# Kernel optimization log

Measured on AMD Instinct MI355X. Metric: run time of the kernel, lower is better.

## Reference

```python
import jax, jax.numpy as jnp
import numpy as np

N = 50000
IN_FEATS = 128
H_FEATS = 256
E = 800000


def setup_inputs() -> dict:
    key = jax.random.key(0)
    ks = jax.random.split(key, 8)
    x = jax.random.normal(ks[0], (N, IN_FEATS), dtype=jnp.float32)
    edge_index = jax.random.randint(ks[1], (2, E), 0, N, dtype=jnp.int64)
    s1 = 1.0 / np.sqrt(IN_FEATS)
    s2 = 1.0 / np.sqrt(H_FEATS)
    # PyG SAGEConv: lin_l (applied to aggregated neighbors, with bias), lin_r (root, no bias)
    W1_l = jax.random.uniform(ks[2], (H_FEATS, IN_FEATS), jnp.float32, -s1, s1)
    b1_l = jax.random.uniform(ks[3], (H_FEATS,), jnp.float32, -s1, s1)
    W1_r = jax.random.uniform(ks[4], (H_FEATS, IN_FEATS), jnp.float32, -s1, s1)
    W2_l = jax.random.uniform(ks[5], (1, H_FEATS), jnp.float32, -s2, s2)
    b2_l = jax.random.uniform(ks[6], (1,), jnp.float32, -s2, s2)
    W2_r = jax.random.uniform(ks[7], (1, H_FEATS), jnp.float32, -s2, s2)
    return {"x": x, "edge_index": edge_index, "W1_l": W1_l, "b1_l": b1_l,
            "W1_r": W1_r, "W2_l": W2_l, "b2_l": b2_l, "W2_r": W2_r}


def _mean_aggregate(feat, src, dst, n_nodes):
    # scatter-mean of source features onto destination nodes
    summed = jax.ops.segment_sum(feat[src], dst, num_segments=n_nodes)
    deg = jax.ops.segment_sum(jnp.ones((src.shape[0],), feat.dtype), dst,
                              num_segments=n_nodes)
    return summed / jnp.maximum(deg, 1.0)[:, None]


def reference(x, edge_index, W1_l, b1_l, W1_r, W2_l, b2_l, W2_r):
    src, dst = edge_index[0], edge_index[1]
    n = x.shape[0]
    # SAGEConv 1: lin_l(mean_agg(x)) + lin_r(x), then ReLU (dropout is identity at eval)
    agg1 = _mean_aggregate(x, src, dst, n)
    h = jax.nn.relu(agg1 @ W1_l.T + b1_l + x @ W1_r.T)
    # SAGEConv 2 -> scalar per node
    agg2 = _mean_aggregate(h, src, dst, n)
    out = (agg2 @ W2_l.T + b2_l + h @ W2_r.T).reshape(-1)
    return out
```

## Files before the change

### kernel.cpp

```cpp
#include <hip/hip_runtime.h>

static constexpr int IN_F   = 128;
static constexpr int ECH    = 4096;
static constexpr int RSLOT  = 64;
static constexpr int CAPB   = 5376;
static constexpr int CSR_CAP = 5376;
static constexpr int OVF_CAP = 4096;

typedef __attribute__((ext_vector_type(8))) short bf16x8;
typedef __attribute__((ext_vector_type(8))) unsigned short u16x8;
typedef __attribute__((ext_vector_type(4))) float f32x4;

__device__ inline unsigned short f2bf(float f) {
    unsigned u = __float_as_uint(f);
    u += 0x7FFF + ((u >> 16) & 1);
    return (unsigned short)(u >> 16);
}
__device__ inline float bf2f(unsigned short h) {
    return __uint_as_float(((unsigned)h) << 16);
}

__global__ __launch_bounds__(256) void edge_bin(const int* __restrict__ src,
        const int* __restrict__ dst, unsigned* __restrict__ btmp,
        int* __restrict__ rcnt, int* __restrict__ ovf_cnt, unsigned* __restrict__ ovf,
        int E) {
    __shared__ unsigned stage[ECH];
    __shared__ int h[256], lcur[256];
    int tid = threadIdx.x, eb = blockIdx.x;
    int base = eb * ECH;
    h[tid] = 0; lcur[tid] = 0;
    __syncthreads();
#pragma unroll
    for (int r = 0; r < ECH / 256; r++) {
        int e = base + r * 256 + tid;
        if (e < E) {
            unsigned d = (unsigned)dst[e];
            stage[r * 256 + tid] = (d << 16) | (unsigned)src[e];
            atomicAdd(&h[d >> 8], 1);
        }
    }
    __syncthreads();
    int hv = h[tid];
    rcnt[eb * 256 + tid] = hv < RSLOT ? hv : RSLOT;
#pragma unroll
    for (int r = 0; r < ECH / 256; r++) {
        int e = base + r * 256 + tid;
        if (e < E) {
            unsigned pk = stage[r * 256 + tid];
            int bkt = pk >> 24;
            int rank = atomicAdd(&lcur[bkt], 1);
            if (rank < RSLOT)
                btmp[(size_t)(eb * 256 + bkt) * RSLOT + rank] = pk;
            else {
                int pos = atomicAdd(ovf_cnt, 1);
                if (pos < OVF_CAP) ovf[pos] = pk;
            }
        }
    }
}

__global__ __launch_bounds__(256) void bucket_csr(const unsigned* __restrict__ btmp,
        const int* __restrict__ rcnt, const int* __restrict__ ovf_cnt,
        const unsigned* __restrict__ ovf,
        int* __restrict__ rowbeg, int* __restrict__ degn, int* __restrict__ col,
        int n, int nblk) {
    __shared__ unsigned stage[CSR_CAP];
    __shared__ unsigned colL[CSR_CAP];
    __shared__ int cntL[256], curL[256];
    __shared__ int ws[4];
    __shared__ int s_extra;
    int b = blockIdx.x, tid = threadIdx.x, lane = tid & 63, wid = tid >> 6;

    int rc = (tid < nblk) ? rcnt[tid * 256 + b] : 0;
    int val = rc;
#pragma unroll
    for (int off = 1; off < 64; off <<= 1) {
        int t = __shfl_up(val, off);
        if (lane >= off) val += t;
    }
    if (lane == 63) ws[wid] = val;
    if (tid == 0) s_extra = 0;
    cntL[tid] = 0;
    __syncthreads();
    int pre = 0;
    for (int w = 0; w < wid; w++) pre += ws[w];
    int rb  = pre + val - rc;
    int cnt = ws[0] + ws[1] + ws[2] + ws[3];
    if (tid < nblk && rc > 0) {
        const unsigned* sp = btmp + (size_t)(tid * 256 + b) * RSLOT;
        for (int i = 0; i < rc; i++) stage[rb + i] = sp[i];
    }
    __syncthreads();
    int novf = *ovf_cnt;
    if (novf > 0) {
        if (novf > OVF_CAP) novf = OVF_CAP;
        for (int i = tid; i < novf; i += 256) {
            unsigned pk = ovf[i];
            if ((int)(pk >> 24) == b) {
                int pos = atomicAdd(&s_extra, 1);
                if (cnt + pos < CSR_CAP) stage[cnt + pos] = pk;
            }
        }
    }
    __syncthreads();
    cnt += s_extra;
    if (cnt > CSR_CAP) cnt = CSR_CAP;
    for (int i = tid; i < cnt; i += 256) atomicAdd(&cntL[(stage[i] >> 16) & 255], 1);
    __syncthreads();
    int v = cntL[tid];
    int val2 = v;
#pragma unroll
    for (int off = 1; off < 64; off <<= 1) {
        int t = __shfl_up(val2, off);
        if (lane >= off) val2 += t;
    }
    if (lane == 63) ws[wid] = val2;
    __syncthreads();
    pre = 0;
    for (int w = 0; w < wid; w++) pre += ws[w];
    int ex = pre + val2 - v;
    curL[tid] = ex;
    int node = b * 256 + tid;
    if (node < n) { rowbeg[node] = b * CAPB + ex; degn[node] = v; }
    __syncthreads();
    for (int i = tid; i < cnt; i += 256) {
        unsigned pk = stage[i];
        int pos = atomicAdd(&curL[(pk >> 16) & 255], 1);
        colL[pos] = pk & 0xFFFFu;
    }
    __syncthreads();
    for (int i = tid; i < cnt; i += 256) col[b * CAPB + i] = (int)colL[i];
}

__global__ __launch_bounds__(256) void split_xw(const float* __restrict__ x,
        const float* __restrict__ W1l, const float* __restrict__ W1r,
        unsigned short* __restrict__ xh,
        unsigned short* __restrict__ Wh, unsigned short* __restrict__ Wl,
        long long total2) {
    long long i = (long long)blockIdx.x * 256 + threadIdx.x;
    if (i < total2) {
        float2 v = ((const float2*)x)[i];
        ((ushort2*)xh)[i] = make_ushort2(f2bf(v.x), f2bf(v.y));
    } else {
        long long wi = i - total2;
        if (wi < 65536) {
            int feat = (int)(wi >> 8), k = (int)(wi & 255);
            float w = (k < IN_F) ? W1l[feat * IN_F + k] : W1r[feat * IN_F + (k - IN_F)];
            unsigned short h = f2bf(w);
            Wh[wi] = h;
            Wl[wi] = f2bf(w - bf2f(h));
        }
    }
}

__global__ void agg1_kernel(const unsigned short* __restrict__ xh,
                            const int* __restrict__ rowbeg, const int* __restrict__ degn,
                            const int* __restrict__ col,
                            unsigned short* __restrict__ aggh, int n) {
    int gid  = blockIdx.x * blockDim.x + threadIdx.x;
    int node = gid >> 5;
    int l32  = threadIdx.x & 31;
    if (node >= n) return;
    int beg = rowbeg[node], dg = degn[node], end = beg + dg;
    float a0 = 0.f, a1 = 0.f, a2 = 0.f, a3 = 0.f;
    int j = beg;
    for (; j + 3 < end; j += 4) {
        int4 cs = *(const int4*)(col + j);
        ushort4 v0 = ((const ushort4*)(xh + (size_t)cs.x * IN_F))[l32];
        ushort4 v1 = ((const ushort4*)(xh + (size_t)cs.y * IN_F))[l32];
        ushort4 v2 = ((const ushort4*)(xh + (size_t)cs.z * IN_F))[l32];
        ushort4 v3 = ((const ushort4*)(xh + (size_t)cs.w * IN_F))[l32];
        a0 += bf2f(v0.x) + bf2f(v1.x) + bf2f(v2.x) + bf2f(v3.x);
        a1 += bf2f(v0.y) + bf2f(v1.y) + bf2f(v2.y) + bf2f(v3.y);
        a2 += bf2f(v0.z) + bf2f(v1.z) + bf2f(v2.z) + bf2f(v3.z);
        a3 += bf2f(v0.w) + bf2f(v1.w) + bf2f(v2.w) + bf2f(v3.w);
    }
    for (; j < end; j++) {
        ushort4 v0 = ((const ushort4*)(xh + (size_t)col[j] * IN_F))[l32];
        a0 += bf2f(v0.x); a1 += bf2f(v0.y); a2 += bf2f(v0.z); a3 += bf2f(v0.w);
    }
    float inv = 1.0f / fmaxf((float)dg, 1.0f);
    ushort4 hi;
    hi.x = f2bf(a0 * inv); hi.y = f2bf(a1 * inv);
    hi.z = f2bf(a2 * inv); hi.w = f2bf(a3 * inv);
    ((ushort4*)(aggh + (size_t)node * IN_F))[l32] = hi;
}

__global__ __launch_bounds__(256, 2) void layer1_kernel(
        const unsigned short* __restrict__ xh,
        const unsigned short* __restrict__ aggh,
        const unsigned short* __restrict__ Wh, const unsigned short* __restrict__ Wl,
        const float* __restrict__ b1l,
        const float* __restrict__ W2l, const float* __restrict__ W2r,
        float* __restrict__ p, float* __restrict__ q, int n) {
    __shared__ unsigned short Ah[128 * 32];
    __shared__ unsigned short Bh[256 * 32];
    __shared__ unsigned short Bl[256 * 32];

    int tid  = threadIdx.x;
    int lane = tid & 63;
    int wv   = tid >> 6;
    int m15  = lane & 15;
    int quad = lane >> 4;
    int node0 = blockIdx.x * 128;

    f32x4 acc[2][16];
#pragma unroll
    for (int nt = 0; nt < 2; nt++)
#pragma unroll
        for (int ft = 0; ft < 16; ft++) acc[nt][ft] = (f32x4){0.f, 0.f, 0.f, 0.f};

    int rown = tid >> 2;
    int sub  = tid & 3;

    for (int kc = 0; kc < 8; kc++) {
        int k0 = kc * 32;
        const unsigned short* Ahs = (kc < 4) ? aggh : xh;
        int aoff = (kc < 4) ? k0 : (k0 - IN_F);

#pragma unroll
        for (int ps = 0; ps < 2; ps++) {
            int nl = ps * 64 + rown;
            int g  = node0 + nl;
            u16x8 hv = {0,0,0,0,0,0,0,0};
            if (g < n) hv = *(const u16x8*)(Ahs + (size_t)g * IN_F + aoff + sub * 8);
            *(u16x8*)&Ah[nl * 32 + sub * 8] = hv;
        }
#pragma unroll
        for (int ps = 0; ps < 4; ps++) {
            int feat = ps * 64 + rown;
            size_t go = (size_t)feat * 256 + k0 + sub * 8;
            *(u16x8*)&Bh[feat * 32 + sub * 8] = *(const u16x8*)(Wh + go);
            *(u16x8*)&Bl[feat * 32 + sub * 8] = *(const u16x8*)(Wl + go);
        }
        __syncthreads();

        bf16x8 a0h = *(const bf16x8*)&Ah[(wv * 32 + m15) * 32 + quad * 8];
        bf16x8 a1h = *(const bf16x8*)&Ah[(wv * 32 + 16 + m15) * 32 + quad * 8];
#pragma unroll
        for (int ft = 0; ft < 16; ft++) {
            bf16x8 bh = *(const bf16x8*)&Bh[(ft * 16 + m15) * 32 + quad * 8];
            bf16x8 bl = *(const bf16x8*)&Bl[(ft * 16 + m15) * 32 + quad * 8];
            acc[0][ft] = __builtin_amdgcn_mfma_f32_16x16x32_bf16(a0h, bh, acc[0][ft], 0, 0, 0);
            acc[0][ft] = __builtin_amdgcn_mfma_f32_16x16x32_bf16(a0h, bl, acc[0][ft], 0, 0, 0);
            acc[1][ft] = __builtin_amdgcn_mfma_f32_16x16x32_bf16(a1h, bh, acc[1][ft], 0, 0, 0);
            acc[1][ft] = __builtin_amdgcn_mfma_f32_16x16x32_bf16(a1h, bl, acc[1][ft], 0, 0, 0);
        }
        __syncthreads();
    }

#pragma unroll
    for (int nt = 0; nt < 2; nt++) {
        float u0 = 0, u1 = 0, u2 = 0, u3 = 0;
        float v0 = 0, v1 = 0, v2 = 0, v3 = 0;
#pragma unroll
        for (int ft = 0; ft < 16; ft++) {
            int fj = ft * 16 + m15;
            float bb = b1l[fj], wl = W2l[fj], wr = W2r[fj];
            f32x4 c = acc[nt][ft];
            float h0 = fmaxf(c[0] + bb, 0.f);
            float h1 = fmaxf(c[1] + bb, 0.f);
            float h2 = fmaxf(c[2] + bb, 0.f);
            float h3 = fmaxf(c[3] + bb, 0.f);
            u0 += h0 * wl; v0 += h0 * wr;
            u1 += h1 * wl; v1 += h1 * wr;
            u2 += h2 * wl; v2 += h2 * wr;
            u3 += h3 * wl; v3 += h3 * wr;
        }
#pragma unroll
        for (int off = 1; off < 16; off <<= 1) {
            u0 += __shfl_xor(u0, off); v0 += __shfl_xor(v0, off);
            u1 += __shfl_xor(u1, off); v1 += __shfl_xor(v1, off);
            u2 += __shfl_xor(u2, off); v2 += __shfl_xor(v2, off);
            u3 += __shfl_xor(u3, off); v3 += __shfl_xor(v3, off);
        }
        if (m15 == 0) {
            int nb = node0 + wv * 32 + nt * 16 + quad * 4;
            if (nb + 0 < n) { p[nb + 0] = u0; q[nb + 0] = v0; }
            if (nb + 1 < n) { p[nb + 1] = u1; q[nb + 1] = v1; }
            if (nb + 2 < n) { p[nb + 2] = u2; q[nb + 2] = v2; }
            if (nb + 3 < n) { p[nb + 3] = u3; q[nb + 3] = v3; }
        }
    }
}

__global__ void out_kernel(const float* __restrict__ p, const float* __restrict__ q,
                           const int* __restrict__ rowbeg, const int* __restrict__ degn,
                           const int* __restrict__ col,
                           const float* __restrict__ b2l,
                           float* __restrict__ out, int n) {
    int gid  = blockIdx.x * blockDim.x + threadIdx.x;
    int node = gid >> 4;
    int l    = threadIdx.x & 15;
    if (node >= n) return;
    int beg = rowbeg[node], dg = degn[node], end = beg + dg;
    float s = 0.f;
    for (int j = beg + l; j < end; j += 16) s += p[col[j]];
#pragma unroll
    for (int off = 8; off; off >>= 1) s += __shfl_xor(s, off);
    if (l == 0) {
        float inv = 1.0f / fmaxf((float)dg, 1.0f);
        out[node] = s * inv + b2l[0] + q[node];
    }
}

extern "C" void kernel_launch(void* const* d_in, const int* in_sizes, int n_in,
                              void* d_out, int out_size, void* d_ws, size_t ws_size,
                              hipStream_t stream) {
    const float* x   = (const float*)d_in[0];
    const int*   ei  = (const int*)  d_in[1];
    const float* W1l = (const float*)d_in[2];
    const float* b1l = (const float*)d_in[3];
    const float* W1r = (const float*)d_in[4];
    const float* W2l = (const float*)d_in[5];
    const float* b2l = (const float*)d_in[6];
    const float* W2r = (const float*)d_in[7];
    float* out = (float*)d_out;

    int n = in_sizes[0] / IN_F;
    int E = in_sizes[1] / 2;
    const int* src = ei;
    const int* dst = ei + E;

    size_t n_pad = ((size_t)n + 256) & ~(size_t)255;
    int nbk  = (n + 255) >> 8;
    int nblk = (E + ECH - 1) / ECH;

    int* ovf_cnt   = (int*)d_ws;
    unsigned* ovf  = (unsigned*)(ovf_cnt + 64);
    int* rcnt      = (int*)(ovf + OVF_CAP);
    int* rowbeg    = rcnt + 65536;
    int* degn      = rowbeg + n_pad;
    unsigned* btmp = (unsigned*)(degn + n_pad);
    int* col       = (int*)(btmp + (size_t)nblk * 256 * RSLOT);
    unsigned short* Whs = (unsigned short*)(col + (size_t)nbk * CAPB + 192);
    unsigned short* Wls  = Whs + 65536;
    unsigned short* xh   = Wls + 65536;
    unsigned short* aggh = xh + (size_t)n * IN_F;
    float* p = (float*)(aggh + (size_t)n * IN_F);
    float* q = p + n_pad;

    hipMemsetAsync(ovf_cnt, 0, sizeof(int), stream);

    edge_bin<<<nblk, 256, 0, stream>>>(src, dst, btmp, rcnt, ovf_cnt, ovf, E);
    bucket_csr<<<nbk, 256, 0, stream>>>(btmp, rcnt, ovf_cnt, ovf,
                                        rowbeg, degn, col, n, nblk);

    long long total2 = (long long)n * IN_F / 2;
    long long tot = total2 + 65536;
    split_xw<<<(int)((tot + 255) / 256), 256, 0, stream>>>(
        x, W1l, W1r, xh, Whs, Wls, total2);

    agg1_kernel<<<(int)(((size_t)n * 32 + 255) / 256), 256, 0, stream>>>(
        xh, rowbeg, degn, col, aggh, n);

    layer1_kernel<<<(n + 127) / 128, 256, 0, stream>>>(
        xh, aggh, Whs, Wls, b1l, W2l, W2r, p, q, n);

    out_kernel<<<(int)(((size_t)n * 16 + 255) / 256), 256, 0, stream>>>(
        p, q, rowbeg, degn, col, b2l, out, n);
}
```

Before: 167.1 us.

## Fuse neighbor aggregation into layer-1 GEMM and merge edge binning with bf16 split

Layer-1 mean aggregation now runs inside the GEMM kernel: each block gathers neighbor rows for its 128 nodes into padded shared memory and feeds the MFMA loop from there, so the aggh intermediate is never written to or read back from global memory. The edge-binning and x/W bf16 conversion kernels are merged into one launch with block-index dispatch, saving a launch and letting the two independent jobs overlap. As a trade-off, the gather now runs at the GEMM kernel's occupancy (launch bounds 256,2, extra ~35KB LDS), so latency hiding for the random gathers may drop.

```diff
diff --git a/kernel.cpp b/kernel.cpp
--- a/kernel.cpp
+++ b/kernel.cpp
@@ -6,6 +6,7 @@
 static constexpr int CAPB   = 5376;
 static constexpr int CSR_CAP = 5376;
 static constexpr int OVF_CAP = 4096;
+static constexpr int ASTR   = 136;
 
 typedef __attribute__((ext_vector_type(8))) short bf16x8;
 typedef __attribute__((ext_vector_type(8))) unsigned short u16x8;
@@ -20,40 +21,63 @@
     return __uint_as_float(((unsigned)h) << 16);
 }
 
-__global__ __launch_bounds__(256) void edge_bin(const int* __restrict__ src,
+__global__ __launch_bounds__(256) void prep_kernel(const int* __restrict__ src,
         const int* __restrict__ dst, unsigned* __restrict__ btmp,
         int* __restrict__ rcnt, int* __restrict__ ovf_cnt, unsigned* __restrict__ ovf,
-        int E) {
+        int E, int nblk,
+        const float* __restrict__ x,
+        const float* __restrict__ W1l, const float* __restrict__ W1r,
+        unsigned short* __restrict__ xh,
+        unsigned short* __restrict__ Wh, unsigned short* __restrict__ Wl,
+        long long total2) {
     __shared__ unsigned stage[ECH];
     __shared__ int h[256], lcur[256];
-    int tid = threadIdx.x, eb = blockIdx.x;
-    int base = eb * ECH;
-    h[tid] = 0; lcur[tid] = 0;
-    __syncthreads();
-#pragma unroll
-    for (int r = 0; r < ECH / 256; r++) {
-        int e = base + r * 256 + tid;
-        if (e < E) {
-            unsigned d = (unsigned)dst[e];
-            stage[r * 256 + tid] = (d << 16) | (unsigned)src[e];
-            atomicAdd(&h[d >> 8], 1);
-        }
-    }
-    __syncthreads();
-    int hv = h[tid];
-    rcnt[eb * 256 + tid] = hv < RSLOT ? hv : RSLOT;
-#pragma unroll
-    for (int r = 0; r < ECH / 256; r++) {
-        int e = base + r * 256 + tid;
-        if (e < E) {
-            unsigned pk = stage[r * 256 + tid];
-            int bkt = pk >> 24;
-            int rank = atomicAdd(&lcur[bkt], 1);
-            if (rank < RSLOT)
-                btmp[(size_t)(eb * 256 + bkt) * RSLOT + rank] = pk;
-            else {
-                int pos = atomicAdd(ovf_cnt, 1);
-                if (pos < OVF_CAP) ovf[pos] = pk;
+    int tid = threadIdx.x;
+    if ((int)blockIdx.x < nblk) {
+        int eb = blockIdx.x;
+        int base = eb * ECH;
+        h[tid] = 0; lcur[tid] = 0;
+        __syncthreads();
+#pragma unroll
+        for (int r = 0; r < ECH / 256; r++) {
+            int e = base + r * 256 + tid;
+            if (e < E) {
+                unsigned d = (unsigned)dst[e];
+                stage[r * 256 + tid] = (d << 16) | (unsigned)src[e];
+                atomicAdd(&h[d >> 8], 1);
+            }
+        }
+        __syncthreads();
+        int hv = h[tid];
+        rcnt[eb * 256 + tid] = hv < RSLOT ? hv : RSLOT;
+#pragma unroll
+        for (int r = 0; r < ECH / 256; r++) {
+            int e = base + r * 256 + tid;
+            if (e < E) {
+                unsigned pk = stage[r * 256 + tid];
+                int bkt = pk >> 24;
+                int rank = atomicAdd(&lcur[bkt], 1);
+                if (rank < RSLOT)
+                    btmp[(size_t)(eb * 256 + bkt) * RSLOT + rank] = pk;
+                else {
+                    int pos = atomicAdd(ovf_cnt, 1);
+                    if (pos < OVF_CAP) ovf[pos] = pk;
+                }
+            }
+        }
+    } else {
+        long long i = (long long)(blockIdx.x - nblk) * 256 + tid;
+        if (i < total2) {
+            float2 v = ((const float2*)x)[i];
+            ((ushort2*)xh)[i] = make_ushort2(f2bf(v.x), f2bf(v.y));
+        } else {
+            long long wi = i - total2;
+            if (wi < 65536) {
+                int feat = (int)(wi >> 8), k = (int)(wi & 255);
+                float w = (k < IN_F) ? W1l[feat * IN_F + k] : W1r[feat * IN_F + (k - IN_F)];
+                unsigned short hh = f2bf(w);
+                Wh[wi] = hh;
+                Wl[wi] = f2bf(w - bf2f(hh));
             }
         }
     }
@@ -132,67 +156,15 @@
     for (int i = tid; i < cnt; i += 256) col[b * CAPB + i] = (int)colL[i];
 }
 
-__global__ __launch_bounds__(256) void split_xw(const float* __restrict__ x,
-        const float* __restrict__ W1l, const float* __restrict__ W1r,
-        unsigned short* __restrict__ xh,
-        unsigned short* __restrict__ Wh, unsigned short* __restrict__ Wl,
-        long long total2) {
-    long long i = (long long)blockIdx.x * 256 + threadIdx.x;
-    if (i < total2) {
-        float2 v = ((const float2*)x)[i];
-        ((ushort2*)xh)[i] = make_ushort2(f2bf(v.x), f2bf(v.y));
-    } else {
-        long long wi = i - total2;
-        if (wi < 65536) {
-            int feat = (int)(wi >> 8), k = (int)(wi & 255);
-            float w = (k < IN_F) ? W1l[feat * IN_F + k] : W1r[feat * IN_F + (k - IN_F)];
-            unsigned short h = f2bf(w);
-            Wh[wi] = h;
-            Wl[wi] = f2bf(w - bf2f(h));
-        }
-    }
-}
-
-__global__ void agg1_kernel(const unsigned short* __restrict__ xh,
-                            const int* __restrict__ rowbeg, const int* __restrict__ degn,
-                            const int* __restrict__ col,
-                            unsigned short* __restrict__ aggh, int n) {
-    int gid  = blockIdx.x * blockDim.x + threadIdx.x;
-    int node = gid >> 5;
-    int l32  = threadIdx.x & 31;
-    if (node >= n) return;
-    int beg = rowbeg[node], dg = degn[node], end = beg + dg;
-    float a0 = 0.f, a1 = 0.f, a2 = 0.f, a3 = 0.f;
-    int j = beg;
-    for (; j + 3 < end; j += 4) {
-        int4 cs = *(const int4*)(col + j);
-        ushort4 v0 = ((const ushort4*)(xh + (size_t)cs.x * IN_F))[l32];
-        ushort4 v1 = ((const ushort4*)(xh + (size_t)cs.y * IN_F))[l32];
-        ushort4 v2 = ((const ushort4*)(xh + (size_t)cs.z * IN_F))[l32];
-        ushort4 v3 = ((const ushort4*)(xh + (size_t)cs.w * IN_F))[l32];
-        a0 += bf2f(v0.x) + bf2f(v1.x) + bf2f(v2.x) + bf2f(v3.x);
-        a1 += bf2f(v0.y) + bf2f(v1.y) + bf2f(v2.y) + bf2f(v3.y);
-        a2 += bf2f(v0.z) + bf2f(v1.z) + bf2f(v2.z) + bf2f(v3.z);
-        a3 += bf2f(v0.w) + bf2f(v1.w) + bf2f(v2.w) + bf2f(v3.w);
-    }
-    for (; j < end; j++) {
-        ushort4 v0 = ((const ushort4*)(xh + (size_t)col[j] * IN_F))[l32];
-        a0 += bf2f(v0.x); a1 += bf2f(v0.y); a2 += bf2f(v0.z); a3 += bf2f(v0.w);
-    }
-    float inv = 1.0f / fmaxf((float)dg, 1.0f);
-    ushort4 hi;
-    hi.x = f2bf(a0 * inv); hi.y = f2bf(a1 * inv);
-    hi.z = f2bf(a2 * inv); hi.w = f2bf(a3 * inv);
-    ((ushort4*)(aggh + (size_t)node * IN_F))[l32] = hi;
-}
-
-__global__ __launch_bounds__(256, 2) void layer1_kernel(
+__global__ __launch_bounds__(256, 2) void fused_l1(
         const unsigned short* __restrict__ xh,
-        const unsigned short* __restrict__ aggh,
+        const int* __restrict__ rowbeg, const int* __restrict__ degn,
+        const int* __restrict__ col,
         const unsigned short* __restrict__ Wh, const unsigned short* __restrict__ Wl,
         const float* __restrict__ b1l,
         const float* __restrict__ W2l, const float* __restrict__ W2r,
         float* __restrict__ p, float* __restrict__ q, int n) {
+    __shared__ unsigned short Aagg[128 * ASTR];
     __shared__ unsigned short Ah[128 * 32];
     __shared__ unsigned short Bh[256 * 32];
     __shared__ unsigned short Bl[256 * 32];
@@ -204,6 +176,41 @@
     int quad = lane >> 4;
     int node0 = blockIdx.x * 128;
 
+    {
+        int half = lane >> 5, l32 = lane & 31;
+#pragma unroll 1
+        for (int i = 0; i < 16; i++) {
+            int nl = wv * 32 + 2 * i + half;
+            int g  = node0 + nl;
+            float a0 = 0.f, a1 = 0.f, a2 = 0.f, a3 = 0.f;
+            if (g < n) {
+                int beg = rowbeg[g], dg = degn[g], end = beg + dg;
+                int j = beg;
+                for (; j + 3 < end; j += 4) {
+                    int4 cs = *(const int4*)(col + j);
+                    ushort4 v0 = ((const ushort4*)(xh + (size_t)cs.x * IN_F))[l32];
+                    ushort4 v1 = ((const ushort4*)(xh + (size_t)cs.y * IN_F))[l32];
+                    ushort4 v2 = ((const ushort4*)(xh + (size_t)cs.z * IN_F))[l32];
+                    ushort4 v3 = ((const ushort4*)(xh + (size_t)cs.w * IN_F))[l32];
+                    a0 += bf2f(v0.x) + bf2f(v1.x) + bf2f(v2.x) + bf2f(v3.x);
+                    a1 += bf2f(v0.y) + bf2f(v1.y) + bf2f(v2.y) + bf2f(v3.y);
+                    a2 += bf2f(v0.z) + bf2f(v1.z) + bf2f(v2.z) + bf2f(v3.z);
+                    a3 += bf2f(v0.w) + bf2f(v1.w) + bf2f(v2.w) + bf2f(v3.w);
+                }
+                for (; j < end; j++) {
+                    ushort4 v0 = ((const ushort4*)(xh + (size_t)col[j] * IN_F))[l32];
+                    a0 += bf2f(v0.x); a1 += bf2f(v0.y);
+                    a2 += bf2f(v0.z); a3 += bf2f(v0.w);
+                }
+                float inv = 1.0f / fmaxf((float)dg, 1.0f);
+                a0 *= inv; a1 *= inv; a2 *= inv; a3 *= inv;
+            }
+            ushort4 hi;
+            hi.x = f2bf(a0); hi.y = f2bf(a1); hi.z = f2bf(a2); hi.w = f2bf(a3);
+            *(ushort4*)&Aagg[nl * ASTR + l32 * 4] = hi;
+        }
+    }
+
     f32x4 acc[2][16];
 #pragma unroll
     for (int nt = 0; nt < 2; nt++)
@@ -215,16 +222,16 @@
 
     for (int kc = 0; kc < 8; kc++) {
         int k0 = kc * 32;
-        const unsigned short* Ahs = (kc < 4) ? aggh : xh;
-        int aoff = (kc < 4) ? k0 : (k0 - IN_F);
-
-#pragma unroll
-        for (int ps = 0; ps < 2; ps++) {
-            int nl = ps * 64 + rown;
-            int g  = node0 + nl;
-            u16x8 hv = {0,0,0,0,0,0,0,0};
-            if (g < n) hv = *(const u16x8*)(Ahs + (size_t)g * IN_F + aoff + sub * 8);
-            *(u16x8*)&Ah[nl * 32 + sub * 8] = hv;
+        if (kc >= 4) {
+            int aoff = k0 - IN_F;
+#pragma unroll
+            for (int ps = 0; ps < 2; ps++) {
+                int nl = ps * 64 + rown;
+                int g  = node0 + nl;
+                u16x8 hv = {0,0,0,0,0,0,0,0};
+                if (g < n) hv = *(const u16x8*)(xh + (size_t)g * IN_F + aoff + sub * 8);
+                *(u16x8*)&Ah[nl * 32 + sub * 8] = hv;
+            }
         }
 #pragma unroll
         for (int ps = 0; ps < 4; ps++) {
@@ -235,8 +242,14 @@
         }
         __syncthreads();
 
-        bf16x8 a0h = *(const bf16x8*)&Ah[(wv * 32 + m15) * 32 + quad * 8];
-        bf16x8 a1h = *(const bf16x8*)&Ah[(wv * 32 + 16 + m15) * 32 + quad * 8];
+        bf16x8 a0h, a1h;
+        if (kc < 4) {
+            a0h = *(const bf16x8*)&Aagg[(wv * 32 + m15) * ASTR + k0 + quad * 8];
+            a1h = *(const bf16x8*)&Aagg[(wv * 32 + 16 + m15) * ASTR + k0 + quad * 8];
+        } else {
+            a0h = *(const bf16x8*)&Ah[(wv * 32 + m15) * 32 + quad * 8];
+            a1h = *(const bf16x8*)&Ah[(wv * 32 + 16 + m15) * 32 + quad * 8];
+        }
 #pragma unroll
         for (int ft = 0; ft < 16; ft++) {
             bf16x8 bh = *(const bf16x8*)&Bh[(ft * 16 + m15) * 32 + quad * 8];
@@ -336,26 +349,22 @@
     unsigned short* Whs = (unsigned short*)(col + (size_t)nbk * CAPB + 192);
     unsigned short* Wls  = Whs + 65536;
     unsigned short* xh   = Wls + 65536;
-    unsigned short* aggh = xh + (size_t)n * IN_F;
-    float* p = (float*)(aggh + (size_t)n * IN_F);
+    float* p = (float*)(xh + (size_t)n * IN_F);
     float* q = p + n_pad;
 
     hipMemsetAsync(ovf_cnt, 0, sizeof(int), stream);
 
-    edge_bin<<<nblk, 256, 0, stream>>>(src, dst, btmp, rcnt, ovf_cnt, ovf, E);
+    long long total2 = (long long)n * IN_F / 2;
+    int split_blocks = (int)((total2 + 65536 + 255) / 256);
+    prep_kernel<<<nblk + split_blocks, 256, 0, stream>>>(
+        src, dst, btmp, rcnt, ovf_cnt, ovf, E, nblk,
+        x, W1l, W1r, xh, Whs, Wls, total2);
+
     bucket_csr<<<nbk, 256, 0, stream>>>(btmp, rcnt, ovf_cnt, ovf,
                                         rowbeg, degn, col, n, nblk);
 
-    long long total2 = (long long)n * IN_F / 2;
-    long long tot = total2 + 65536;
-    split_xw<<<(int)((tot + 255) / 256), 256, 0, stream>>>(
-        x, W1l, W1r, xh, Whs, Wls, total2);
-
-    agg1_kernel<<<(int)(((size_t)n * 32 + 255) / 256), 256, 0, stream>>>(
-        xh, rowbeg, degn, col, aggh, n);
-
-    layer1_kernel<<<(n + 127) / 128, 256, 0, stream>>>(
-        xh, aggh, Whs, Wls, b1l, W2l, W2r, p, q, n);
+    fused_l1<<<(n + 127) / 128, 256, 0, stream>>>(
+        xh, rowbeg, degn, col, Whs, Wls, b1l, W2l, W2r, p, q, n);
 
     out_kernel<<<(int)(((size_t)n * 16 + 255) / 256), 256, 0, stream>>>(
         p, q, rowbeg, degn, col, b2l, out, n);
```

Measured after the change: 205.8 us. 1.23x slower.
